# Performance work log

Measured on AMD Instinct MI355X. Metric: run time of the kernel, lower is better.

## Reference

```python
import jax, jax.numpy as jnp
import numpy as np

N_NODES = 100000
N_EDGES = 20000
NNZ = 600000
N_GRAPHS = 64
IN_C, HID_C, OUT_C = 128, 128, 16


def setup_inputs() -> dict:
    key = jax.random.key(0)
    ks = jax.random.split(key, 10)
    x = jax.random.normal(ks[0], (N_NODES, IN_C), dtype=jnp.float32)
    node_idx = jax.random.randint(ks[1], (NNZ,), 0, N_NODES)
    edge_idx = jax.random.randint(ks[2], (NNZ,), 0, N_EDGES)
    batch = jnp.sort(jax.random.randint(ks[3], (N_NODES,), 0, N_GRAPHS))
    s1 = 1.0 / np.sqrt(IN_C)
    s2 = 1.0 / np.sqrt(HID_C)
    W1 = jax.random.uniform(ks[4], (IN_C, HID_C), jnp.float32, -s1, s1)
    b1 = jnp.zeros((HID_C,), jnp.float32)
    W2 = jax.random.uniform(ks[5], (HID_C, HID_C), jnp.float32, -s2, s2)
    b2 = jnp.zeros((HID_C,), jnp.float32)
    Wfc = jax.random.uniform(ks[6], (HID_C, OUT_C), jnp.float32, -s2, s2)
    bfc = jax.random.uniform(ks[7], (OUT_C,), jnp.float32, -s2, s2)
    return {"x": x, "node_idx": node_idx, "edge_idx": edge_idx, "batch": batch,
            "W1": W1, "b1": b1, "W2": W2, "b2": b2, "Wfc": Wfc, "bfc": bfc}


def hypergraph_conv(x, node_idx, edge_idx, W, b):
    # x' = D^{-1} H B^{-1} H^T (x W) + b   (unit hyperedge weights)
    x = x @ W  # lin has bias=False in PyG HypergraphConv
    ones = jnp.ones((node_idx.shape[0],), x.dtype)
    De = jax.ops.segment_sum(ones, edge_idx, num_segments=N_EDGES)   # hyperedge degree
    Dn = jax.ops.segment_sum(ones, node_idx, num_segments=N_NODES)  # node degree
    Binv = jnp.where(De > 0, 1.0 / De, 0.0)[:, None]
    Dinv = jnp.where(Dn > 0, 1.0 / Dn, 0.0)[:, None]
    # node -> hyperedge aggregation
    e = jax.ops.segment_sum(x[node_idx], edge_idx, num_segments=N_EDGES) * Binv
    # hyperedge -> node aggregation
    out = jax.ops.segment_sum(e[edge_idx], node_idx, num_segments=N_NODES) * Dinv
    return out + b


def reference(x, node_idx, edge_idx, batch, W1, b1, W2, b2, Wfc, bfc):
    h = jax.nn.relu(hypergraph_conv(x, node_idx, edge_idx, W1, b1))
    h = jax.nn.relu(hypergraph_conv(h, node_idx, edge_idx, W2, b2))
    # global mean pool over graphs
    cnt = jax.ops.segment_sum(jnp.ones((N_NODES,), h.dtype), batch, num_segments=N_GRAPHS)
    pooled = jax.ops.segment_sum(h, batch, num_segments=N_GRAPHS) / jnp.maximum(cnt, 1.0)[:, None]
    logits = pooled @ Wfc + bfc
    return jax.nn.log_softmax(logits, axis=1)
```

## Files before the change

### kernel.cpp

```cpp
#include <hip/hip_runtime.h>

#define N_NODES  100000
#define N_EDGES  20000
#define NNZ_     600000
#define N_GRAPHS 64
#define C_       128

typedef unsigned short ushort_t;
typedef unsigned int   uint_t;
typedef unsigned char  uchar_t;
typedef __attribute__((ext_vector_type(8))) short bf16x8;
typedef __attribute__((ext_vector_type(8))) unsigned short u16x8;
typedef __attribute__((ext_vector_type(4))) float f32x4;
typedef __attribute__((ext_vector_type(2))) float f32x2;

__device__ __forceinline__ ushort_t f2bf(float f) {
    uint_t u = __float_as_uint(f);
    u += 0x7fffu + ((u >> 16) & 1u);
    return (ushort_t)(u >> 16);
}
__device__ __forceinline__ uint_t pkbf(float lo, float hi) {
    return ((uint_t)f2bf(hi) << 16) | f2bf(lo);
}


#define SORT_ITEMS 2048
#define BKT_CAP    16384
#define NBKT_E     40
#define NBKT_N     49
#define HIST_E_SPLIT 8
#define HIST_N_SPLIT 4
#define NB_E 20
#define NB_N 98

__global__ __launch_bounds__(256) void scatter1(const int* __restrict__ node_idx,
                                                const int* __restrict__ edge_idx,
                                                int* __restrict__ bcur,
                                                int2* __restrict__ stage_e,
                                                int2* __restrict__ stage_n) {
    __shared__ int cnt[NBKT_N];
    __shared__ int base[NBKT_N];
    __shared__ int gbase[NBKT_N];
    __shared__ int2 buf[SORT_ITEMS];
    int t = threadIdx.x;
    int start = blockIdx.x * SORT_ITEMS;
    int nitems = min(SORT_ITEMS, NNZ_ - start);

    int ek[8], nk[8];
    #pragma unroll
    for (int j = 0; j < 8; j++) {
        int i = t + j * 256;
        if (i < nitems) { ek[j] = edge_idx[start + i]; nk[j] = node_idx[start + i]; }
    }

    #pragma unroll
    for (int side = 0; side < 2; side++) {
        const int SHIFT = side ? 11 : 9;
        const int NBKT  = side ? NBKT_N : NBKT_E;
        int2* stage = side ? stage_n : stage_e;
        int*  bc    = bcur + side * 64;

        if (side) __syncthreads();
        for (int i = t; i < NBKT; i += 256) cnt[i] = 0;
        __syncthreads();

        int rank[8], bkt[8];
        #pragma unroll
        for (int j = 0; j < 8; j++) {
            int i = t + j * 256;
            if (i < nitems) {
                int key = side ? nk[j] : ek[j];
                bkt[j]  = key >> SHIFT;
                rank[j] = atomicAdd(&cnt[bkt[j]], 1);
            }
        }
        __syncthreads();
        if (t < 64) {
            int v = (t < NBKT) ? cnt[t] : 0;
            int s = v;
            #pragma unroll
            for (int o = 1; o < 64; o <<= 1) { int u = __shfl_up(s, o); if (t >= o) s += u; }
            if (t < NBKT) base[t] = s - v;
        }
        __syncthreads();
        if (t < NBKT) {
            int c = cnt[t];
            gbase[t] = t * BKT_CAP + ((c > 0) ? atomicAdd(&bc[t], c) : 0);
        }
        #pragma unroll
        for (int j = 0; j < 8; j++) {
            int i = t + j * 256;
            if (i < nitems) {
                int key = side ? nk[j] : ek[j];
                int val = side ? ek[j] : nk[j];
                buf[base[bkt[j]] + rank[j]] = make_int2(key, val);
            }
        }
        __syncthreads();
        for (int i = t; i < nitems; i += 256) {
            int2 p = buf[i];
            int b = p.x >> SHIFT;
            stage[gbase[b] + (i - base[b])] = p;
        }
    }
}

__global__ __launch_bounds__(256) void hist_both(const int2* __restrict__ stage_e,
                                                 const int2* __restrict__ stage_n,
                                                 const int* __restrict__ bcur,
                                                 int* __restrict__ ecnt, int* __restrict__ ncnt) {
    __shared__ int hist[2048];
    int bx = blockIdx.x;
    if (bx < NBKT_E * HIST_E_SPLIT) {
        int b = bx / HIST_E_SPLIT, sp = bx % HIST_E_SPLIT;
        const int2* stage = stage_e + (size_t)b * BKT_CAP;
        int n = bcur[b];
        int per = (n + HIST_E_SPLIT - 1) / HIST_E_SPLIT;
        int ss = sp * per, ee = min(ss + per, n);
        for (int i = threadIdx.x; i < 512; i += 256) hist[i] = 0;
        __syncthreads();
        int k0 = b << 9;
        for (int i = ss + threadIdx.x; i < ee; i += 256) atomicAdd(&hist[stage[i].x - k0], 1);
        __syncthreads();
        for (int i = threadIdx.x; i < 512; i += 256) {
            int k = k0 + i;
            if (k < N_EDGES) atomicAdd(&ecnt[k], hist[i]);
        }
    } else {
        bx -= NBKT_E * HIST_E_SPLIT;
        int b = bx / HIST_N_SPLIT, sp = bx % HIST_N_SPLIT;
        const int2* stage = stage_n + (size_t)b * BKT_CAP;
        int n = bcur[64 + b];
        int per = (n + HIST_N_SPLIT - 1) / HIST_N_SPLIT;
        int ss = sp * per, ee = min(ss + per, n);
        for (int i = threadIdx.x; i < 2048; i += 256) hist[i] = 0;
        __syncthreads();
        int k0 = b << 11;
        for (int i = ss + threadIdx.x; i < ee; i += 256) atomicAdd(&hist[stage[i].x - k0], 1);
        __syncthreads();
        for (int i = threadIdx.x; i < 2048; i += 256) {
            int k = k0 + i;
            if (k < N_NODES) atomicAdd(&ncnt[k], hist[i]);
        }
    }
}


__device__ __forceinline__ int block_incl_scan_256(int v, int* lds) {
    int t = threadIdx.x;
    lds[t] = v; __syncthreads();
    #pragma unroll
    for (int o = 1; o < 256; o <<= 1) {
        int u = (t >= o) ? lds[t - o] : 0;
        __syncthreads();
        v += u;
        lds[t] = v;
        __syncthreads();
    }
    return v;
}

__global__ __launch_bounds__(256) void scan_part_both(const int* __restrict__ ecnt,
                                                      const int* __restrict__ ncnt,
                                                      int* __restrict__ bsum) {
    __shared__ int lds[256];
    int bx = blockIdx.x;
    const int* in; int n, bb; int* bs;
    if (bx < NB_E) { in = ecnt; n = N_EDGES; bb = bx; bs = bsum; }
    else           { in = ncnt; n = N_NODES; bb = bx - NB_E; bs = bsum + 512; }
    int base = bb * 1024 + threadIdx.x * 4;
    int s = 0;
    #pragma unroll
    for (int j = 0; j < 4; j++) s += (base + j < n) ? in[base + j] : 0;
    int incl = block_incl_scan_256(s, lds);
    if (threadIdx.x == 255) bs[bb] = incl;
}

__global__ __launch_bounds__(256) void scan_sums_both(int* __restrict__ bsum) {
    __shared__ int lds[256];
    int* bs = bsum + blockIdx.x * 512;
    int nb  = blockIdx.x ? NB_N : NB_E;
    int t = threadIdx.x;
    int v = (t < nb) ? bs[t] : 0;
    int incl = block_incl_scan_256(v, lds);
    if (t < nb) bs[t] = incl - v;
}

__global__ __launch_bounds__(256) void scan_write_both(const int* __restrict__ ecnt,
                                                       const int* __restrict__ ncnt,
                                                       const int* __restrict__ bsum,
                                                       int* __restrict__ eoffs, int* __restrict__ noffs,
                                                       float* __restrict__ binv, float* __restrict__ dinv) {
    __shared__ int lds[256];
    int bx = blockIdx.x;
    const int* in; int n, bb; const int* bs; int* out; float* inv;
    if (bx < NB_E) { in = ecnt; n = N_EDGES; bb = bx;        bs = bsum;       out = eoffs; inv = binv; }
    else           { in = ncnt; n = N_NODES; bb = bx - NB_E; bs = bsum + 512; out = noffs; inv = dinv; }
    int base = bb * 1024 + threadIdx.x * 4;
    int x[4];
    int ts = 0;
    #pragma unroll
    for (int j = 0; j < 4; j++) { x[j] = (base + j < n) ? in[base + j] : 0; ts += x[j]; }
    int incl = block_incl_scan_256(ts, lds);
    int run = bs[bb] + (incl - ts);
    #pragma unroll
    for (int j = 0; j < 4; j++) {
        if (base + j < n) {
            out[base + j] = run;
            inv[base + j] = (x[j] > 0) ? 1.0f / (float)x[j] : 0.0f;
        }
        run += x[j];
    }
}

__global__ __launch_bounds__(1024) void fill_lds(const int2* __restrict__ stage_e,
                                                 const int2* __restrict__ stage_n,
                                                 const int* __restrict__ bcur,
                                                 const int* __restrict__ eoffs,
                                                 const int* __restrict__ noffs,
                                                 int* __restrict__ csr_en,
                                                 int* __restrict__ csr_ne) {
    __shared__ int cur[2048];
    int bx = blockIdx.x;
    const int2* sb; const int* koffs; int* csr; int n, k0, width, nkeys;
    if (bx < NBKT_E) {
        sb = stage_e + (size_t)bx * BKT_CAP; koffs = eoffs; csr = csr_en;
        n = bcur[bx]; k0 = bx << 9; width = 512; nkeys = N_EDGES;
    } else {
        int b = bx - NBKT_E;
        sb = stage_n + (size_t)b * BKT_CAP; koffs = noffs; csr = csr_ne;
        n = bcur[64 + b]; k0 = b << 11; width = 2048; nkeys = N_NODES;
    }
    int base = koffs[k0];
    for (int i = threadIdx.x; i < width; i += 1024) {
        int k = k0 + i;
        cur[i] = (k < nkeys) ? (koffs[k] - base) : 0;
    }
    __syncthreads();
    for (int i = threadIdx.x; i < n; i += 1024) {
        int2 p = sb[i];
        int pos = atomicAdd(&cur[p.x - k0], 1);
        csr[base + pos] = p.y;
    }
}


#define CONV_XBLKS 6250

__global__ __launch_bounds__(256) void conv_all(const float* __restrict__ X, uint_t* __restrict__ X8,
                                                const float* __restrict__ W1, const float* __restrict__ W2,
                                                ushort_t* __restrict__ WT1, ushort_t* __restrict__ WT2) {
    int bx = blockIdx.x;
    if (bx < CONV_XBLKS) {
        size_t c = (size_t)bx * 256 + threadIdx.x;
        size_t base = c * 8;
        if (base >= (size_t)N_NODES * C_) return;
        float4 f0 = *(const float4*)(X + base);
        float4 f1 = *(const float4*)(X + base + 4);
        uint_t w0 = 0, w1 = 0;
        w0 = __builtin_amdgcn_cvt_pk_fp8_f32(f0.x, f0.y, w0, 0);
        w0 = __builtin_amdgcn_cvt_pk_fp8_f32(f0.z, f0.w, w0, 1);
        w1 = __builtin_amdgcn_cvt_pk_fp8_f32(f1.x, f1.y, w1, 0);
        w1 = __builtin_amdgcn_cvt_pk_fp8_f32(f1.z, f1.w, w1, 1);
        uint2 o; o.x = w0; o.y = w1;
        *(uint2*)(X8 + c * 2) = o;
    } else {
        bx -= CONV_XBLKS;
        const float* W = (bx < 64) ? W1 : W2;
        ushort_t* WT   = (bx < 64) ? WT1 : WT2;
        int idx = (bx & 63) * 256 + threadIdx.x;
        int n = idx >> 7, k = idx & 127;
        WT[n * 128 + k] = f2bf(W[k * 128 + n]);
    }
}


__global__ __launch_bounds__(256) void gemm_mfma(const ushort_t* __restrict__ Ab,
                                                 const ushort_t* __restrict__ WT,
                                                 uchar_t* __restrict__ C8, int M) {
    __shared__ __align__(16) ushort_t Wl[128 * 128];
    __shared__ __align__(16) ushort_t Al[64 * 128];
    int t = threadIdx.x;
    int r0 = blockIdx.x * 64;

    const uint4* WTg = (const uint4*)WT;
    #pragma unroll
    for (int i = 0; i < 8; i++) {
        int c = i * 256 + t;
        int row = c >> 4, colel = (c & 15) * 8;
        *(uint4*)&Wl[row * 128 + (colel ^ ((row & 7) << 3))] = WTg[c];
    }
    #pragma unroll
    for (int i = 0; i < 4; i++) {
        int c = i * 256 + t;
        int row = c >> 4;
        int colel = (c & 15) * 8;
        int gr = r0 + row; if (gr >= M) gr = M - 1;
        u16x8 v = *(const u16x8*)(Ab + (size_t)gr * 128 + colel);
        *(u16x8*)&Al[row * 128 + (colel ^ ((row & 7) << 3))] = v;
    }
    __syncthreads();

    int lane = t & 63, wid = t >> 6;
    int arow = wid * 16 + (lane & 15);
    int kq = lane >> 4;
    f32x4 acc[8] = {};

    #pragma unroll
    for (int ks = 0; ks < 4; ks++) {
        int colel = ks * 32 + kq * 8;
        bf16x8 a = *(const bf16x8*)&Al[arow * 128 + (colel ^ ((arow & 7) << 3))];
        #pragma unroll
        for (int nt = 0; nt < 8; nt++) {
            int wr = nt * 16 + (lane & 15);
            bf16x8 b = *(const bf16x8*)&Wl[wr * 128 + (colel ^ ((wr & 7) << 3))];
            acc[nt] = __builtin_amdgcn_mfma_f32_16x16x32_bf16(a, b, acc[nt], 0, 0, 0);
        }
    }

    __syncthreads();
    uchar_t* Cl = (uchar_t*)Al;
    #pragma unroll
    for (int nt = 0; nt < 8; nt++) {
        int col = nt * 16 + (lane & 15);
        #pragma unroll
        for (int j = 0; j < 4; j++) {
            int rl = wid * 16 + kq * 4 + j;
            uint_t p = __builtin_amdgcn_cvt_pk_fp8_f32(acc[nt][j], acc[nt][j], 0, 0);
            Cl[rl * 128 + col] = (uchar_t)(p & 0xff);
        }
    }
    __syncthreads();
    int rows_here = min(64, M - r0);
    uint4* dst = (uint4*)(C8 + (size_t)r0 * 128);
    const uint4* src = (const uint4*)Cl;
    for (int c = t; c < rows_here * 8; c += 256) dst[c] = src[c];
}


__device__ __forceinline__ void acc16(uint4 v, float* a) {
    f32x2 p0 = __builtin_amdgcn_cvt_pk_f32_fp8(v.x, 0);
    f32x2 p1 = __builtin_amdgcn_cvt_pk_f32_fp8(v.x, 1);
    f32x2 p2 = __builtin_amdgcn_cvt_pk_f32_fp8(v.y, 0);
    f32x2 p3 = __builtin_amdgcn_cvt_pk_f32_fp8(v.y, 1);
    f32x2 p4 = __builtin_amdgcn_cvt_pk_f32_fp8(v.z, 0);
    f32x2 p5 = __builtin_amdgcn_cvt_pk_f32_fp8(v.z, 1);
    f32x2 p6 = __builtin_amdgcn_cvt_pk_f32_fp8(v.w, 0);
    f32x2 p7 = __builtin_amdgcn_cvt_pk_f32_fp8(v.w, 1);
    a[0] += p0.x;  a[1] += p0.y;  a[2] += p1.x;  a[3] += p1.y;
    a[4] += p2.x;  a[5] += p2.y;  a[6] += p3.x;  a[7] += p3.y;
    a[8] += p4.x;  a[9] += p4.y;  a[10] += p5.x; a[11] += p5.y;
    a[12] += p6.x; a[13] += p6.y; a[14] += p7.x; a[15] += p7.y;
}

__global__ __launch_bounds__(256) void gather_edges8(const uint4* __restrict__ X,
                                                     const int* __restrict__ csr,
                                                     const int* __restrict__ off, const int* __restrict__ cnt,
                                                     const float* __restrict__ binv,
                                                     ushort_t* __restrict__ E) {
    int g = (blockIdx.x * blockDim.x + threadIdx.x) >> 3;
    int l = threadIdx.x & 7;
    if (g >= N_EDGES) return;
    int s = off[g], n = cnt[g];
    float a[16] = {};
    int i = 0;
    for (; i + 4 <= n; i += 4) {
        int r0 = csr[s + i], r1 = csr[s + i + 1], r2 = csr[s + i + 2], r3 = csr[s + i + 3];
        uint4 v0 = X[(size_t)r0 * 8 + l];
        uint4 v1 = X[(size_t)r1 * 8 + l];
        uint4 v2 = X[(size_t)r2 * 8 + l];
        uint4 v3 = X[(size_t)r3 * 8 + l];
        acc16(v0, a); acc16(v1, a); acc16(v2, a); acc16(v3, a);
    }
    for (; i < n; i++) {
        uint4 v = X[(size_t)csr[s + i] * 8 + l];
        acc16(v, a);
    }
    float sc = binv[g];
    uint4 o0, o1;
    o0.x = pkbf(a[0] * sc,  a[1] * sc);
    o0.y = pkbf(a[2] * sc,  a[3] * sc);
    o0.z = pkbf(a[4] * sc,  a[5] * sc);
    o0.w = pkbf(a[6] * sc,  a[7] * sc);
    o1.x = pkbf(a[8] * sc,  a[9] * sc);
    o1.y = pkbf(a[10] * sc, a[11] * sc);
    o1.z = pkbf(a[12] * sc, a[13] * sc);
    o1.w = pkbf(a[14] * sc, a[15] * sc);
    uint4* dst = (uint4*)(E + (size_t)g * 128) + l * 2;
    dst[0] = o0; dst[1] = o1;
}

__global__ __launch_bounds__(256) void gather_nodes8(const uint4* __restrict__ F,
                                                     const int* __restrict__ csr,
                                                     const int* __restrict__ off, const int* __restrict__ cnt,
                                                     const float* __restrict__ dinv,
                                                     const float* __restrict__ bias,
                                                     uint4* __restrict__ Y) {
    int g = (blockIdx.x * blockDim.x + threadIdx.x) >> 3;
    int l = threadIdx.x & 7;
    if (g >= N_NODES) return;
    int s = off[g], n = cnt[g];
    float a[16] = {};
    int i = 0;
    for (; i + 4 <= n; i += 4) {
        int r0 = csr[s + i], r1 = csr[s + i + 1], r2 = csr[s + i + 2], r3 = csr[s + i + 3];
        uint4 v0 = F[(size_t)r0 * 8 + l];
        uint4 v1 = F[(size_t)r1 * 8 + l];
        uint4 v2 = F[(size_t)r2 * 8 + l];
        uint4 v3 = F[(size_t)r3 * 8 + l];
        acc16(v0, a); acc16(v1, a); acc16(v2, a); acc16(v3, a);
    }
    for (; i < n; i++) {
        uint4 v = F[(size_t)csr[s + i] * 8 + l];
        acc16(v, a);
    }
    float sc = dinv[g];
    const float4* bb = (const float4*)bias + l * 4;
    float4 b0 = bb[0], b1 = bb[1], b2 = bb[2], b3 = bb[3];
    float r[16];
    r[0]  = fmaxf(a[0]  * sc + b0.x, 0.f);
    r[1]  = fmaxf(a[1]  * sc + b0.y, 0.f);
    r[2]  = fmaxf(a[2]  * sc + b0.z, 0.f);
    r[3]  = fmaxf(a[3]  * sc + b0.w, 0.f);
    r[4]  = fmaxf(a[4]  * sc + b1.x, 0.f);
    r[5]  = fmaxf(a[5]  * sc + b1.y, 0.f);
    r[6]  = fmaxf(a[6]  * sc + b1.z, 0.f);
    r[7]  = fmaxf(a[7]  * sc + b1.w, 0.f);
    r[8]  = fmaxf(a[8]  * sc + b2.x, 0.f);
    r[9]  = fmaxf(a[9]  * sc + b2.y, 0.f);
    r[10] = fmaxf(a[10] * sc + b2.z, 0.f);
    r[11] = fmaxf(a[11] * sc + b2.w, 0.f);
    r[12] = fmaxf(a[12] * sc + b3.x, 0.f);
    r[13] = fmaxf(a[13] * sc + b3.y, 0.f);
    r[14] = fmaxf(a[14] * sc + b3.z, 0.f);
    r[15] = fmaxf(a[15] * sc + b3.w, 0.f);
    uint_t w0 = __builtin_amdgcn_cvt_pk_fp8_f32(r[0],  r[1],  0, 0);
    w0 = __builtin_amdgcn_cvt_pk_fp8_f32(r[2],  r[3],  w0, 1);
    uint_t w1 = __builtin_amdgcn_cvt_pk_fp8_f32(r[4],  r[5],  0, 0);
    w1 = __builtin_amdgcn_cvt_pk_fp8_f32(r[6],  r[7],  w1, 1);
    uint_t w2 = __builtin_amdgcn_cvt_pk_fp8_f32(r[8],  r[9],  0, 0);
    w2 = __builtin_amdgcn_cvt_pk_fp8_f32(r[10], r[11], w2, 1);
    uint_t w3 = __builtin_amdgcn_cvt_pk_fp8_f32(r[12], r[13], 0, 0);
    w3 = __builtin_amdgcn_cvt_pk_fp8_f32(r[14], r[15], w3, 1);
    uint4 o; o.x = w0; o.y = w1; o.z = w2; o.w = w3;
    Y[(size_t)g * 8 + l] = o;
}


#define POOL_BLOCKS 1024

__global__ __launch_bounds__(256) void pool_kernel8(const ushort_t* __restrict__ H,
                                                    const int* __restrict__ batch,
                                                    float* __restrict__ P) {
    int wgid = blockIdx.x * 4 + (threadIdx.x >> 6);
    int lane = threadIdx.x & 63;
    const int NW = POOL_BLOCKS * 4;
    const int per = (N_NODES + NW - 1) / NW;
    int r0 = wgid * per;
    int r1 = min(r0 + per, N_NODES);
    if (r0 >= r1) return;
    float ax = 0.f, ay = 0.f;
    int g = batch[r0];
    int hiw = lane & 1;
    for (int r = r0; r < r1; r++) {
        int gr = batch[r];
        if (gr != g) {
            atomicAdd(&P[g * C_ + lane * 2],     ax);
            atomicAdd(&P[g * C_ + lane * 2 + 1], ay);
            ax = 0.f; ay = 0.f; g = gr;
        }
        uint_t v = ((const uint_t*)H)[(size_t)r * 32 + (lane >> 1)];
        f32x2 p = hiw ? __builtin_amdgcn_cvt_pk_f32_fp8(v, 1)
                      : __builtin_amdgcn_cvt_pk_f32_fp8(v, 0);
        ax += p.x; ay += p.y;
    }
    atomicAdd(&P[g * C_ + lane * 2],     ax);
    atomicAdd(&P[g * C_ + lane * 2 + 1], ay);
}

__device__ __forceinline__ int lower_bound_dev(const int* __restrict__ a, int n, int key) {
    int lo = 0, hi = n;
    while (lo < hi) { int mid = (lo + hi) >> 1; if (a[mid] < key) lo = mid + 1; else hi = mid; }
    return lo;
}

__global__ __launch_bounds__(1024) void final_kernel(const float* __restrict__ P, const int* __restrict__ batch,
                                                     const float* __restrict__ Wfc, const float* __restrict__ bfc,
                                                     float* __restrict__ out) {
    int t = threadIdx.x;
    int r = t >> 4, c = t & 15;
    int lo = lower_bound_dev(batch, N_NODES, r);
    int hi = lower_bound_dev(batch, N_NODES, r + 1);
    float cnt = (float)((hi - lo) > 0 ? (hi - lo) : 1);
    float acc = 0.f;
    #pragma unroll 8
    for (int k = 0; k < C_; k++) acc += P[r * C_ + k] * Wfc[k * 16 + c];
    float logit = acc / cnt + bfc[c];
    __shared__ float l[N_GRAPHS][16];
    l[r][c] = logit;
    __syncthreads();
    float m = -1e30f;
    #pragma unroll
    for (int k = 0; k < 16; k++) m = fmaxf(m, l[r][k]);
    float sum = 0.f;
    #pragma unroll
    for (int k = 0; k < 16; k++) sum += expf(l[r][k] - m);
    out[t] = logit - m - logf(sum);
}


extern "C" void kernel_launch(void* const* d_in, const int* in_sizes, int n_in,
                              void* d_out, int out_size, void* d_ws, size_t ws_size,
                              hipStream_t stream) {
    const float* x        = (const float*)d_in[0];
    const int*   node_idx = (const int*)  d_in[1];
    const int*   edge_idx = (const int*)  d_in[2];
    const int*   batch    = (const int*)  d_in[3];
    const float* W1       = (const float*)d_in[4];
    const float* b1       = (const float*)d_in[5];
    const float* W2       = (const float*)d_in[6];
    const float* b2       = (const float*)d_in[7];
    const float* Wfc      = (const float*)d_in[8];
    const float* bfc      = (const float*)d_in[9];
    float* out = (float*)d_out;

    char* ws = (char*)d_ws;
    size_t off = 0;
    auto alloc = [&](size_t bytes) -> char* {
        off = (off + 255) & ~(size_t)255;
        char* p = ws + off;
        off += bytes;
        return p;
    };

    uint_t* x8     = (uint_t*)  alloc((size_t)N_NODES * C_);
    uint_t* h8     = (uint_t*)  alloc((size_t)N_NODES * C_);
    ushort_t* Eb   = (ushort_t*)alloc((size_t)N_EDGES * C_ * 2);
    uchar_t* Fb8   = (uchar_t*) alloc((size_t)N_EDGES * C_);
    ushort_t* wt1  = (ushort_t*)alloc((size_t)C_ * C_ * 2);
    ushort_t* wt2  = (ushort_t*)alloc((size_t)C_ * C_ * 2);
    int2*  stage_e = (int2*) alloc((size_t)NBKT_E * BKT_CAP * 8);
    int2*  stage_n = (int2*) alloc((size_t)NBKT_N * BKT_CAP * 8);
    int*   ecnt   = (int*)  alloc((size_t)N_EDGES * 4);
    int*   ncnt   = (int*)  alloc((size_t)N_NODES * 4);
    int*   bcur   = (int*)  alloc((size_t)128 * 4);
    float* pooled = (float*)alloc((size_t)N_GRAPHS * C_ * 4);
    char*  zend   = ws + off;
    int*   eoffs  = (int*)  alloc((size_t)N_EDGES * 4);
    int*   noffs  = (int*)  alloc((size_t)N_NODES * 4);
    int*   csr_en = (int*)  alloc((size_t)NNZ_ * 4);
    int*   csr_ne = (int*)  alloc((size_t)NNZ_ * 4);
    float* binv   = (float*)alloc((size_t)N_EDGES * 4);
    float* dinv   = (float*)alloc((size_t)N_NODES * 4);
    int*   bsum   = (int*)  alloc((size_t)1024 * 4);

    (void)hipMemsetAsync((void*)ecnt, 0, (size_t)(zend - (char*)ecnt), stream);

    const int SB = (NNZ_ + SORT_ITEMS - 1) / SORT_ITEMS;
    scatter1<<<SB, 256, 0, stream>>>(node_idx, edge_idx, bcur, stage_e, stage_n);
    hist_both<<<NBKT_E * HIST_E_SPLIT + NBKT_N * HIST_N_SPLIT, 256, 0, stream>>>(
        stage_e, stage_n, bcur, ecnt, ncnt);
    scan_part_both <<<NB_E + NB_N, 256, 0, stream>>>(ecnt, ncnt, bsum);
    scan_sums_both <<<2, 256, 0, stream>>>(bsum);
    scan_write_both<<<NB_E + NB_N, 256, 0, stream>>>(ecnt, ncnt, bsum, eoffs, noffs, binv, dinv);
    fill_lds<<<NBKT_E + NBKT_N, 1024, 0, stream>>>(stage_e, stage_n, bcur, eoffs, noffs,
                                                   csr_en, csr_ne);

    conv_all<<<CONV_XBLKS + 128, 256, 0, stream>>>(x, x8, W1, W2, wt1, wt2);

    const int GEB = (N_EDGES + 63) / 64;
    gather_edges8<<<N_EDGES * 8 / 256, 256, 0, stream>>>((const uint4*)x8, csr_en, eoffs, ecnt, binv, Eb);
    gemm_mfma<<<GEB, 256, 0, stream>>>(Eb, wt1, Fb8, N_EDGES);
    gather_nodes8<<<N_NODES * 8 / 256, 256, 0, stream>>>((const uint4*)Fb8, csr_ne, noffs, ncnt, dinv, b1,
                                                         (uint4*)h8);
    gather_edges8<<<N_EDGES * 8 / 256, 256, 0, stream>>>((const uint4*)h8, csr_en, eoffs, ecnt, binv, Eb);
    gemm_mfma<<<GEB, 256, 0, stream>>>(Eb, wt2, Fb8, N_EDGES);
    gather_nodes8<<<N_NODES * 8 / 256, 256, 0, stream>>>((const uint4*)Fb8, csr_ne, noffs, ncnt, dinv, b2,
                                                         (uint4*)x8);
    pool_kernel8<<<POOL_BLOCKS, 256, 0, stream>>>((const ushort_t*)x8, batch, pooled);
    final_kernel<<<1, 1024, 0, stream>>>(pooled, batch, Wfc, bfc, out);
}
```

Measured before the change: 178.5 us.

## Fuse CSR build into one per-bucket kernel and merge input conversion with scatter

Replaces the chain of histogram, three-pass scan and fill kernels with one kernel per key bucket. That kernel computes the local histogram in LDS, scans it with wave shuffles, derives the global base from a prefix over bucket counts, and writes counts, offsets, inverse degrees and CSR entries directly. The fp8/bf16 conversion kernel is merged into the scatter kernel's grid, and the memset shrinks to just the bucket counters and the pooled buffer. The aim is to remove about five kernel launches and the global-atomic histogram traffic. In exchange, the CSR build has less parallelism: 89 blocks each process a whole bucket.

```diff
diff --git a/kernel.cpp b/kernel.cpp
--- a/kernel.cpp
+++ b/kernel.cpp
@@ -28,22 +28,51 @@
 #define BKT_CAP    16384
 #define NBKT_E     40
 #define NBKT_N     49
-#define HIST_E_SPLIT 8
-#define HIST_N_SPLIT 4
-#define NB_E 20
-#define NB_N 98
-
-__global__ __launch_bounds__(256) void scatter1(const int* __restrict__ node_idx,
-                                                const int* __restrict__ edge_idx,
-                                                int* __restrict__ bcur,
-                                                int2* __restrict__ stage_e,
-                                                int2* __restrict__ stage_n) {
+#define SB_        ((NNZ_ + SORT_ITEMS - 1) / SORT_ITEMS)
+#define CONV_XBLKS 6250
+
+__global__ __launch_bounds__(256) void scatter_conv(const int* __restrict__ node_idx,
+                                                    const int* __restrict__ edge_idx,
+                                                    int* __restrict__ bcur,
+                                                    int2* __restrict__ stage_e,
+                                                    int2* __restrict__ stage_n,
+                                                    const float* __restrict__ X, uint_t* __restrict__ X8,
+                                                    const float* __restrict__ W1, const float* __restrict__ W2,
+                                                    ushort_t* __restrict__ WT1, ushort_t* __restrict__ WT2) {
     __shared__ int cnt[NBKT_N];
     __shared__ int base[NBKT_N];
     __shared__ int gbase[NBKT_N];
     __shared__ int2 buf[SORT_ITEMS];
     int t = threadIdx.x;
-    int start = blockIdx.x * SORT_ITEMS;
+    int bxx = blockIdx.x;
+
+    if (bxx >= SB_) {
+        int bx = bxx - SB_;
+        if (bx < CONV_XBLKS) {
+            size_t c = (size_t)bx * 256 + t;
+            size_t bb = c * 8;
+            if (bb >= (size_t)N_NODES * C_) return;
+            float4 f0 = *(const float4*)(X + bb);
+            float4 f1 = *(const float4*)(X + bb + 4);
+            uint_t w0 = 0, w1 = 0;
+            w0 = __builtin_amdgcn_cvt_pk_fp8_f32(f0.x, f0.y, w0, 0);
+            w0 = __builtin_amdgcn_cvt_pk_fp8_f32(f0.z, f0.w, w0, 1);
+            w1 = __builtin_amdgcn_cvt_pk_fp8_f32(f1.x, f1.y, w1, 0);
+            w1 = __builtin_amdgcn_cvt_pk_fp8_f32(f1.z, f1.w, w1, 1);
+            uint2 o; o.x = w0; o.y = w1;
+            *(uint2*)(X8 + c * 2) = o;
+        } else {
+            bx -= CONV_XBLKS;
+            const float* W = (bx < 64) ? W1 : W2;
+            ushort_t* WT   = (bx < 64) ? WT1 : WT2;
+            int idx = (bx & 63) * 256 + t;
+            int nn = idx >> 7, k = idx & 127;
+            WT[nn * 128 + k] = f2bf(W[k * 128 + nn]);
+        }
+        return;
+    }
+
+    int start = bxx * SORT_ITEMS;
     int nitems = min(SORT_ITEMS, NNZ_ - start);
 
     int ek[8], nk[8];
@@ -105,172 +134,80 @@
     }
 }
 
-__global__ __launch_bounds__(256) void hist_both(const int2* __restrict__ stage_e,
-                                                 const int2* __restrict__ stage_n,
-                                                 const int* __restrict__ bcur,
-                                                 int* __restrict__ ecnt, int* __restrict__ ncnt) {
+__global__ __launch_bounds__(1024) void bucket_build(const int2* __restrict__ stage_e,
+                                                     const int2* __restrict__ stage_n,
+                                                     const int* __restrict__ bcur,
+                                                     int* __restrict__ ecnt, int* __restrict__ ncnt,
+                                                     int* __restrict__ eoffs, int* __restrict__ noffs,
+                                                     float* __restrict__ binv, float* __restrict__ dinv,
+                                                     int* __restrict__ csr_en, int* __restrict__ csr_ne) {
     __shared__ int hist[2048];
+    __shared__ int offs[2048];
+    __shared__ int wsum[16];
+    __shared__ int sbase;
+    int t = threadIdx.x;
     int bx = blockIdx.x;
-    if (bx < NBKT_E * HIST_E_SPLIT) {
-        int b = bx / HIST_E_SPLIT, sp = bx % HIST_E_SPLIT;
-        const int2* stage = stage_e + (size_t)b * BKT_CAP;
-        int n = bcur[b];
-        int per = (n + HIST_E_SPLIT - 1) / HIST_E_SPLIT;
-        int ss = sp * per, ee = min(ss + per, n);
-        for (int i = threadIdx.x; i < 512; i += 256) hist[i] = 0;
-        __syncthreads();
-        int k0 = b << 9;
-        for (int i = ss + threadIdx.x; i < ee; i += 256) atomicAdd(&hist[stage[i].x - k0], 1);
-        __syncthreads();
-        for (int i = threadIdx.x; i < 512; i += 256) {
-            int k = k0 + i;
-            if (k < N_EDGES) atomicAdd(&ecnt[k], hist[i]);
-        }
+    const int2* sb; int* cnt; int* koffs; float* inv; int* csr;
+    const int* bc; int b, width, nkeys, nb, k0;
+    if (bx < NBKT_E) {
+        b = bx; bc = bcur;
+        sb = stage_e + (size_t)b * BKT_CAP; cnt = ecnt; koffs = eoffs; inv = binv; csr = csr_en;
+        k0 = b << 9; width = 512; nkeys = N_EDGES; nb = NBKT_E;
     } else {
-        bx -= NBKT_E * HIST_E_SPLIT;
-        int b = bx / HIST_N_SPLIT, sp = bx % HIST_N_SPLIT;
-        const int2* stage = stage_n + (size_t)b * BKT_CAP;
-        int n = bcur[64 + b];
-        int per = (n + HIST_N_SPLIT - 1) / HIST_N_SPLIT;
-        int ss = sp * per, ee = min(ss + per, n);
-        for (int i = threadIdx.x; i < 2048; i += 256) hist[i] = 0;
-        __syncthreads();
-        int k0 = b << 11;
-        for (int i = ss + threadIdx.x; i < ee; i += 256) atomicAdd(&hist[stage[i].x - k0], 1);
-        __syncthreads();
-        for (int i = threadIdx.x; i < 2048; i += 256) {
-            int k = k0 + i;
-            if (k < N_NODES) atomicAdd(&ncnt[k], hist[i]);
-        }
-    }
-}
-
-
-__device__ __forceinline__ int block_incl_scan_256(int v, int* lds) {
-    int t = threadIdx.x;
-    lds[t] = v; __syncthreads();
-    #pragma unroll
-    for (int o = 1; o < 256; o <<= 1) {
-        int u = (t >= o) ? lds[t - o] : 0;
-        __syncthreads();
-        v += u;
-        lds[t] = v;
-        __syncthreads();
-    }
-    return v;
-}
-
-__global__ __launch_bounds__(256) void scan_part_both(const int* __restrict__ ecnt,
-                                                      const int* __restrict__ ncnt,
-                                                      int* __restrict__ bsum) {
-    __shared__ int lds[256];
-    int bx = blockIdx.x;
-    const int* in; int n, bb; int* bs;
-    if (bx < NB_E) { in = ecnt; n = N_EDGES; bb = bx; bs = bsum; }
-    else           { in = ncnt; n = N_NODES; bb = bx - NB_E; bs = bsum + 512; }
-    int base = bb * 1024 + threadIdx.x * 4;
-    int s = 0;
-    #pragma unroll
-    for (int j = 0; j < 4; j++) s += (base + j < n) ? in[base + j] : 0;
-    int incl = block_incl_scan_256(s, lds);
-    if (threadIdx.x == 255) bs[bb] = incl;
-}
-
-__global__ __launch_bounds__(256) void scan_sums_both(int* __restrict__ bsum) {
-    __shared__ int lds[256];
-    int* bs = bsum + blockIdx.x * 512;
-    int nb  = blockIdx.x ? NB_N : NB_E;
-    int t = threadIdx.x;
-    int v = (t < nb) ? bs[t] : 0;
-    int incl = block_incl_scan_256(v, lds);
-    if (t < nb) bs[t] = incl - v;
-}
-
-__global__ __launch_bounds__(256) void scan_write_both(const int* __restrict__ ecnt,
-                                                       const int* __restrict__ ncnt,
-                                                       const int* __restrict__ bsum,
-                                                       int* __restrict__ eoffs, int* __restrict__ noffs,
-                                                       float* __restrict__ binv, float* __restrict__ dinv) {
-    __shared__ int lds[256];
-    int bx = blockIdx.x;
-    const int* in; int n, bb; const int* bs; int* out; float* inv;
-    if (bx < NB_E) { in = ecnt; n = N_EDGES; bb = bx;        bs = bsum;       out = eoffs; inv = binv; }
-    else           { in = ncnt; n = N_NODES; bb = bx - NB_E; bs = bsum + 512; out = noffs; inv = dinv; }
-    int base = bb * 1024 + threadIdx.x * 4;
-    int x[4];
-    int ts = 0;
-    #pragma unroll
-    for (int j = 0; j < 4; j++) { x[j] = (base + j < n) ? in[base + j] : 0; ts += x[j]; }
-    int incl = block_incl_scan_256(ts, lds);
-    int run = bs[bb] + (incl - ts);
-    #pragma unroll
-    for (int j = 0; j < 4; j++) {
-        if (base + j < n) {
-            out[base + j] = run;
-            inv[base + j] = (x[j] > 0) ? 1.0f / (float)x[j] : 0.0f;
-        }
-        run += x[j];
-    }
-}
-
-__global__ __launch_bounds__(1024) void fill_lds(const int2* __restrict__ stage_e,
-                                                 const int2* __restrict__ stage_n,
-                                                 const int* __restrict__ bcur,
-                                                 const int* __restrict__ eoffs,
-                                                 const int* __restrict__ noffs,
-                                                 int* __restrict__ csr_en,
-                                                 int* __restrict__ csr_ne) {
-    __shared__ int cur[2048];
-    int bx = blockIdx.x;
-    const int2* sb; const int* koffs; int* csr; int n, k0, width, nkeys;
-    if (bx < NBKT_E) {
-        sb = stage_e + (size_t)bx * BKT_CAP; koffs = eoffs; csr = csr_en;
-        n = bcur[bx]; k0 = bx << 9; width = 512; nkeys = N_EDGES;
-    } else {
-        int b = bx - NBKT_E;
-        sb = stage_n + (size_t)b * BKT_CAP; koffs = noffs; csr = csr_ne;
-        n = bcur[64 + b]; k0 = b << 11; width = 2048; nkeys = N_NODES;
-    }
-    int base = koffs[k0];
-    for (int i = threadIdx.x; i < width; i += 1024) {
+        b = bx - NBKT_E; bc = bcur + 64;
+        sb = stage_n + (size_t)b * BKT_CAP; cnt = ncnt; koffs = noffs; inv = dinv; csr = csr_ne;
+        k0 = b << 11; width = 2048; nkeys = N_NODES; nb = NBKT_N;
+    }
+    int n = bc[b];
+    if (t < 64) {
+        int v = (t < nb) ? bc[t] : 0;
+        int s = v;
+        #pragma unroll
+        for (int o = 1; o < 64; o <<= 1) { int u = __shfl_up(s, o); if (t >= o) s += u; }
+        if (t == b) sbase = s - v;
+    }
+    for (int i = t; i < width; i += 1024) hist[i] = 0;
+    __syncthreads();
+    for (int i = t; i < n; i += 1024) atomicAdd(&hist[sb[i].x - k0], 1);
+    __syncthreads();
+    int e0 = 0, e1 = 0;
+    if (2 * t < width) { e0 = hist[2 * t]; e1 = hist[2 * t + 1]; }
+    int s = e0 + e1;
+    int lane = t & 63, wv = t >> 6;
+    int sc = s;
+    #pragma unroll
+    for (int o = 1; o < 64; o <<= 1) { int u = __shfl_up(sc, o); if (lane >= o) sc += u; }
+    if (lane == 63) wsum[wv] = sc;
+    __syncthreads();
+    if (t < 16) {
+        int v = wsum[t];
+        int s2 = v;
+        #pragma unroll
+        for (int o = 1; o < 16; o <<= 1) { int u = __shfl_up(s2, o); if (t >= o) s2 += u; }
+        wsum[t] = s2 - v;
+    }
+    __syncthreads();
+    if (2 * t < width) {
+        int excl = (sc - s) + wsum[wv];
+        offs[2 * t]     = excl;
+        offs[2 * t + 1] = excl + e0;
+    }
+    __syncthreads();
+    int base_g = sbase;
+    for (int i = t; i < width; i += 1024) {
         int k = k0 + i;
-        cur[i] = (k < nkeys) ? (koffs[k] - base) : 0;
-    }
-    __syncthreads();
-    for (int i = threadIdx.x; i < n; i += 1024) {
+        if (k < nkeys) {
+            int c = hist[i];
+            cnt[k]   = c;
+            koffs[k] = base_g + offs[i];
+            inv[k]   = (c > 0) ? 1.0f / (float)c : 0.0f;
+        }
+    }
+    __syncthreads();
+    for (int i = t; i < n; i += 1024) {
         int2 p = sb[i];
-        int pos = atomicAdd(&cur[p.x - k0], 1);
-        csr[base + pos] = p.y;
-    }
-}
-
-
-#define CONV_XBLKS 6250
-
-__global__ __launch_bounds__(256) void conv_all(const float* __restrict__ X, uint_t* __restrict__ X8,
-                                                const float* __restrict__ W1, const float* __restrict__ W2,
-                                                ushort_t* __restrict__ WT1, ushort_t* __restrict__ WT2) {
-    int bx = blockIdx.x;
-    if (bx < CONV_XBLKS) {
-        size_t c = (size_t)bx * 256 + threadIdx.x;
-        size_t base = c * 8;
-        if (base >= (size_t)N_NODES * C_) return;
-        float4 f0 = *(const float4*)(X + base);
-        float4 f1 = *(const float4*)(X + base + 4);
-        uint_t w0 = 0, w1 = 0;
-        w0 = __builtin_amdgcn_cvt_pk_fp8_f32(f0.x, f0.y, w0, 0);
-        w0 = __builtin_amdgcn_cvt_pk_fp8_f32(f0.z, f0.w, w0, 1);
-        w1 = __builtin_amdgcn_cvt_pk_fp8_f32(f1.x, f1.y, w1, 0);
-        w1 = __builtin_amdgcn_cvt_pk_fp8_f32(f1.z, f1.w, w1, 1);
-        uint2 o; o.x = w0; o.y = w1;
-        *(uint2*)(X8 + c * 2) = o;
-    } else {
-        bx -= CONV_XBLKS;
-        const float* W = (bx < 64) ? W1 : W2;
-        ushort_t* WT   = (bx < 64) ? WT1 : WT2;
-        int idx = (bx & 63) * 256 + threadIdx.x;
-        int n = idx >> 7, k = idx & 127;
-        WT[n * 128 + k] = f2bf(W[k * 128 + n]);
+        int pos = atomicAdd(&offs[p.x - k0], 1);
+        csr[base_g + pos] = p.y;
     }
 }
 
@@ -541,32 +478,24 @@
     ushort_t* wt2  = (ushort_t*)alloc((size_t)C_ * C_ * 2);
     int2*  stage_e = (int2*) alloc((size_t)NBKT_E * BKT_CAP * 8);
     int2*  stage_n = (int2*) alloc((size_t)NBKT_N * BKT_CAP * 8);
-    int*   ecnt   = (int*)  alloc((size_t)N_EDGES * 4);
-    int*   ncnt   = (int*)  alloc((size_t)N_NODES * 4);
     int*   bcur   = (int*)  alloc((size_t)128 * 4);
     float* pooled = (float*)alloc((size_t)N_GRAPHS * C_ * 4);
     char*  zend   = ws + off;
+    int*   ecnt   = (int*)  alloc((size_t)N_EDGES * 4);
+    int*   ncnt   = (int*)  alloc((size_t)N_NODES * 4);
     int*   eoffs  = (int*)  alloc((size_t)N_EDGES * 4);
     int*   noffs  = (int*)  alloc((size_t)N_NODES * 4);
     int*   csr_en = (int*)  alloc((size_t)NNZ_ * 4);
     int*   csr_ne = (int*)  alloc((size_t)NNZ_ * 4);
     float* binv   = (float*)alloc((size_t)N_EDGES * 4);
     float* dinv   = (float*)alloc((size_t)N_NODES * 4);
-    int*   bsum   = (int*)  alloc((size_t)1024 * 4);
-
-    (void)hipMemsetAsync((void*)ecnt, 0, (size_t)(zend - (char*)ecnt), stream);
-
-    const int SB = (NNZ_ + SORT_ITEMS - 1) / SORT_ITEMS;
-    scatter1<<<SB, 256, 0, stream>>>(node_idx, edge_idx, bcur, stage_e, stage_n);
-    hist_both<<<NBKT_E * HIST_E_SPLIT + NBKT_N * HIST_N_SPLIT, 256, 0, stream>>>(
-        stage_e, stage_n, bcur, ecnt, ncnt);
-    scan_part_both <<<NB_E + NB_N, 256, 0, stream>>>(ecnt, ncnt, bsum);
-    scan_sums_both <<<2, 256, 0, stream>>>(bsum);
-    scan_write_both<<<NB_E + NB_N, 256, 0, stream>>>(ecnt, ncnt, bsum, eoffs, noffs, binv, dinv);
-    fill_lds<<<NBKT_E + NBKT_N, 1024, 0, stream>>>(stage_e, stage_n, bcur, eoffs, noffs,
-                                                   csr_en, csr_ne);
-
-    conv_all<<<CONV_XBLKS + 128, 256, 0, stream>>>(x, x8, W1, W2, wt1, wt2);
+
+    (void)hipMemsetAsync((void*)bcur, 0, (size_t)(zend - (char*)bcur), stream);
+
+    scatter_conv<<<SB_ + CONV_XBLKS + 128, 256, 0, stream>>>(
+        node_idx, edge_idx, bcur, stage_e, stage_n, x, x8, W1, W2, wt1, wt2);
+    bucket_build<<<NBKT_E + NBKT_N, 1024, 0, stream>>>(
+        stage_e, stage_n, bcur, ecnt, ncnt, eoffs, noffs, binv, dinv, csr_en, csr_ne);
 
     const int GEB = (N_EDGES + 63) / 64;
     gather_edges8<<<N_EDGES * 8 / 256, 256, 0, stream>>>((const uint4*)x8, csr_en, eoffs, ecnt, binv, Eb);
```

After: 159.9 us. 10.4% less time.
